# Performance work log

Measured on AMD Instinct MI355X. Metric: run time of the kernel, lower is better.

Reference implementation:

```python
import jax, jax.numpy as jnp
import numpy as np

D_MODEL = 1024
N_HEADS = 16
HEAD_DIM = D_MODEL // N_HEADS
SEQ_LEN = 2048
LN_EPS = 1e-5


def setup_inputs() -> dict:
    key = jax.random.key(0)
    ks = jax.random.split(key, 7)
    s = 1.0 / np.sqrt(D_MODEL)
    h = jax.random.normal(ks[0], (SEQ_LEN, D_MODEL), dtype=jnp.float32)
    # torch nn.Linear weights are (out_features, in_features)
    W_qkv = jax.random.uniform(ks[1], (3 * D_MODEL, D_MODEL), jnp.float32, -s, s)
    b_qkv = jax.random.uniform(ks[2], (3 * D_MODEL,), jnp.float32, -s, s)
    W_out = jax.random.uniform(ks[3], (D_MODEL, D_MODEL), jnp.float32, -s, s)
    b_out = jax.random.uniform(ks[4], (D_MODEL,), jnp.float32, -s, s)
    gamma = jnp.ones((D_MODEL,), jnp.float32)
    beta = jnp.zeros((D_MODEL,), jnp.float32)
    return {"h": h, "W_qkv": W_qkv, "b_qkv": b_qkv, "W_out": W_out,
            "b_out": b_out, "gamma": gamma, "beta": beta}


def reference(h, W_qkv, b_qkv, W_out, b_out, gamma, beta):
    S = h.shape[0]
    # QKV projection: (S, 3*D)
    qkv = h @ W_qkv.T + b_qkv
    q, k, v = jnp.split(qkv, 3, axis=-1)
    # (S, D) -> (H, S, Dh)
    q = q.reshape(S, N_HEADS, HEAD_DIM).transpose(1, 0, 2)
    k = k.reshape(S, N_HEADS, HEAD_DIM).transpose(1, 0, 2)
    v = v.reshape(S, N_HEADS, HEAD_DIM).transpose(1, 0, 2)
    # scaled dot-product attention, non-causal (matches F.sdpa defaults)
    scale = 1.0 / jnp.sqrt(jnp.asarray(HEAD_DIM, dtype=h.dtype))
    scores = jnp.einsum('hqd,hkd->hqk', q, k) * scale  # (H, S, S)
    attn = jax.nn.softmax(scores, axis=-1)
    attn_out = jnp.einsum('hqk,hkd->hqd', attn, v)     # (H, S, Dh)
    attn_out = attn_out.transpose(1, 0, 2).reshape(S, D_MODEL)
    # output projection + residual + LayerNorm
    attn_out = attn_out @ W_out.T + b_out
    x = h + attn_out
    mu = jnp.mean(x, axis=-1, keepdims=True)
    var = jnp.var(x, axis=-1, keepdims=True)
    x_norm = (x - mu) * jax.lax.rsqrt(var + LN_EPS)
    return x_norm * gamma + beta
```

## Files before the change

kernel.cpp:

```cpp
#include <hip/hip_runtime.h>
#include <stdint.h>

#define SEQ 2048
#define DM 1024
#define NH 16
#define DH 64
#define LN_EPS 1e-5f

typedef __bf16 bf16x8 __attribute__((ext_vector_type(8)));
typedef float f32x4 __attribute__((ext_vector_type(4)));
typedef unsigned short u16;
typedef unsigned short u16x8 __attribute__((ext_vector_type(8)));
typedef unsigned int u32;
typedef short s16x4 __attribute__((ext_vector_type(4)));

__device__ __forceinline__ u16 f2bf(float f) {
  unsigned int u = __float_as_uint(f);
  unsigned int r = (u + 0x7fffu + ((u >> 16) & 1u)) >> 16;
  return (u16)r;
}

__device__ __forceinline__ float bf2f(u16 x) {
  return __uint_as_float(((u32)x) << 16);
}

__device__ __forceinline__ u32 packbf(float a, float b) {
  union { __bf16 h[2]; u32 u; } pw;
  pw.h[0] = (__bf16)a; pw.h[1] = (__bf16)b;
  return pw.u;
}

__device__ __forceinline__ float fast_exp2(float x) {
#if __has_builtin(__builtin_amdgcn_exp2f)
  return __builtin_amdgcn_exp2f(x);
#else
  float r;
  asm("v_exp_f32 %0, %1" : "=v"(r) : "v"(x));
  return r;
#endif
}

__device__ __forceinline__ f32x4 mfma16x16x16bf(s16x4 a, s16x4 b, f32x4 c) {
#if __has_builtin(__builtin_amdgcn_mfma_f32_16x16x16bf16_1k)
  return __builtin_amdgcn_mfma_f32_16x16x16bf16_1k(a, b, c, 0, 0, 0);
#else
  asm("v_mfma_f32_16x16x16_bf16 %0, %1, %2, %0" : "+v"(c) : "v"(a), "v"(b));
  return c;
#endif
}

#define GLD_LDS16(gp, lp) __builtin_amdgcn_global_load_lds( \
  (const __attribute__((address_space(1))) void*)(gp),      \
  (__attribute__((address_space(3))) void*)(lp), 16, 0, 0)

__global__ __launch_bounds__(256)
void k_f2bf3(const float* __restrict__ a, u16* __restrict__ oa, int na,
             const float* __restrict__ b, u16* __restrict__ ob, int nb,
             const float* __restrict__ c, u16* __restrict__ oc, int nc) {
  int i = blockIdx.x * 256 + threadIdx.x;
  const float* src;
  u16* dst;
  if (i < na) { src = a; dst = oa; }
  else if (i < na + nb) { src = b; dst = ob; i -= na; }
  else if (i < na + nb + nc) { src = c; dst = oc; i -= na + nb; }
  else return;
  float4 v = reinterpret_cast<const float4*>(src)[i];
  ushort4 o;
  o.x = f2bf(v.x); o.y = f2bf(v.y); o.z = f2bf(v.z); o.w = f2bf(v.w);
  reinterpret_cast<ushort4*>(dst)[i] = o;
}

template <int EPI, int BM, int BN, int XCDW>
__global__ __launch_bounds__(256)
void k_gemm_bt(const u16* __restrict__ A, const u16* __restrict__ B,
               const float* __restrict__ bias,
               u16* __restrict__ outb, u16* __restrict__ outv,
               int M, int N, int K) {
  constexpr int MF = BM / 32, NF = BN / 32;
  constexpr int WM = BM / 2, WN = BN / 2;
  constexpr int NLOAD = BM / 32 + BN / 32;
  __shared__ u16 Alds[2][BM][64];
  __shared__ u16 Blds[2][BN][64];
  const int tid = threadIdx.x;
  const int w = tid >> 6, l = tid & 63, lg = l >> 4, lr = l & 15;
  const int wr = w >> 1, wc = w & 1;

  int bx = blockIdx.x, by = blockIdx.y, bz = blockIdx.z;
  if (XCDW > 0) {
    const int nx = gridDim.x, ny = gridDim.y;
    const int u = bx + nx * (by + ny * bz);
    const int xcd = u & 7, g = u >> 3;
    bx = xcd * XCDW + (g % XCDW);
    const int rem = g / XCDW;
    by = rem % ny;
    bz = rem / ny;
  }

  const int m0 = by * BM, n0 = bx * BN;
  const int KTall = K >> 6;
  const int ktn = KTall / gridDim.z;
  const int kt0 = bz * ktn;

  f32x4 acc[MF][NF] = {};

  const int srow = l >> 3;
  const int scol = ((l & 7) ^ (srow & 7)) * 8;
  auto stage = [&](int buf, int kt) {
    const int k0 = kt << 6;
#pragma unroll
    for (int p = 0; p < BM / 32; ++p) {
      const int rbase = (w * (BM / 32) + p) * 8;
      GLD_LDS16(A + (size_t)(m0 + rbase + srow) * K + k0 + scol, &Alds[buf][rbase][0]);
    }
#pragma unroll
    for (int p = 0; p < BN / 32; ++p) {
      const int rbase = (w * (BN / 32) + p) * 8;
      GLD_LDS16(B + (size_t)(n0 + rbase + srow) * K + k0 + scol, &Blds[buf][rbase][0]);
    }
  };

  auto aread = [&](int buf, int row, int kbyte) -> bf16x8 {
    const int off = row * 128 + (kbyte ^ ((row & 7) << 4));
    return *reinterpret_cast<const bf16x8*>(
        reinterpret_cast<const char*>(&Alds[buf][0][0]) + off);
  };
  auto bread = [&](int buf, int row, int kbyte) -> bf16x8 {
    const int off = row * 128 + (kbyte ^ ((row & 7) << 4));
    return *reinterpret_cast<const bf16x8*>(
        reinterpret_cast<const char*>(&Blds[buf][0][0]) + off);
  };

  auto compute = [&](int buf) {
#pragma unroll
    for (int kk = 0; kk < 2; ++kk) {
      bf16x8 af[MF], bfr[NF];
#pragma unroll
      for (int mi = 0; mi < MF; ++mi)
        af[mi] = aread(buf, wr * WM + mi * 16 + lr, kk * 64 + lg * 16);
#pragma unroll
      for (int ni = 0; ni < NF; ++ni)
        bfr[ni] = bread(buf, wc * WN + ni * 16 + lr, kk * 64 + lg * 16);
#pragma unroll
      for (int mi = 0; mi < MF; ++mi)
#pragma unroll
        for (int ni = 0; ni < NF; ++ni)
          acc[mi][ni] = __builtin_amdgcn_mfma_f32_16x16x32_bf16(af[mi], bfr[ni], acc[mi][ni], 0, 0, 0);
    }
  };

  stage(0, kt0);
  for (int i = 0; i < ktn; ++i) {
    const int cur = i & 1;
    if (i + 1 < ktn) {
      stage(cur ^ 1, kt0 + i + 1);
      if (NLOAD == 6)      asm volatile("s_waitcnt vmcnt(6)" ::: "memory");
      else if (NLOAD == 4) asm volatile("s_waitcnt vmcnt(4)" ::: "memory");
      else                 asm volatile("s_waitcnt vmcnt(0)" ::: "memory");
    } else {
      asm volatile("s_waitcnt vmcnt(0)" ::: "memory");
    }
    __builtin_amdgcn_s_barrier();
    compute(cur);
    __builtin_amdgcn_s_barrier();
  }

  if (EPI == 3) {
    u16* op = outb + (size_t)bz * M * N;
#pragma unroll
    for (int ni = 0; ni < NF; ++ni) {
      const int n = n0 + wc * WN + ni * 16 + lr;
#pragma unroll
      for (int mi = 0; mi < MF; ++mi) {
#pragma unroll
        for (int r = 0; r < 4; ++r) {
          const int m = m0 + wr * WM + mi * 16 + lg * 4 + r;
          op[(size_t)m * N + n] = f2bf(acc[mi][ni][r]);
        }
      }
    }
  } else {
    if (n0 < 2048) {
#pragma unroll
      for (int ni = 0; ni < NF; ++ni) {
        const int n = n0 + wc * WN + ni * 16 + lr;
        const float bn = bias[n];
#pragma unroll
        for (int mi = 0; mi < MF; ++mi) {
#pragma unroll
          for (int r = 0; r < 4; ++r) {
            const int m = m0 + wr * WM + mi * 16 + lg * 4 + r;
            outb[(size_t)m * 2048 + n] = f2bf(acc[mi][ni][r] + bn);
          }
        }
      }
    } else {
#pragma unroll
      for (int ni = 0; ni < NF; ++ni) {
        const int n = n0 + wc * WN + ni * 16 + lr;
        const float bn = bias[n];
#pragma unroll
        for (int mi = 0; mi < MF; ++mi) {
          const int mb = m0 + wr * WM + mi * 16 + lg * 4;
          ushort4 pk;
          pk.x = f2bf(acc[mi][ni][0] + bn);
          pk.y = f2bf(acc[mi][ni][1] + bn);
          pk.z = f2bf(acc[mi][ni][2] + bn);
          pk.w = f2bf(acc[mi][ni][3] + bn);
          *reinterpret_cast<ushort4*>(&outv[(size_t)(n - 2048) * M + mb]) = pk;
        }
      }
    }
  }
}

template <int KSPLIT>
__global__ __launch_bounds__(256)
void k_attn(const u16* __restrict__ qk, const u16* __restrict__ vt,
            u16* __restrict__ Opart, float* __restrict__ lsum_out) {
  __shared__ u16 Klds[2][64 * 64];
  __shared__ u16 Vlds[2][64 * 64];
  const int tid = threadIdx.x;
  const int w = tid >> 6, l = tid & 63, lg = l >> 4, lr = l & 15;

  const int u = blockIdx.x + 16 * (blockIdx.y + NH * blockIdx.z);
  const int xcd = u & 7, g = u >> 3;
  const int h = 2 * xcd + (g / (16 * KSPLIT));
  const int rem = g % (16 * KSPLIT);
  const int sp = rem >> 4;
  const int qb2 = rem & 15;

  constexpr int NT = (SEQ / 64) / KSPLIT;
  const int kb0 = sp * NT;

  bf16x8 qfA[2], qfB[2];
  {
    const size_t qrowA = (size_t)(qb2 * 128 + w * 16 + lr) * 2048 + h * 64;
    qfA[0] = *reinterpret_cast<const bf16x8*>(&qk[qrowA + lg * 8]);
    qfA[1] = *reinterpret_cast<const bf16x8*>(&qk[qrowA + 32 + lg * 8]);
    const size_t qrowB = qrowA + (size_t)64 * 2048;
    qfB[0] = *reinterpret_cast<const bf16x8*>(&qk[qrowB + lg * 8]);
    qfB[1] = *reinterpret_cast<const bf16x8*>(&qk[qrowB + 32 + lg * 8]);
  }

  const int sr0 = w * 16 + (l >> 3);
  const int sc0 = ((l & 7) ^ (sr0 & 7)) * 8;
  const int sr1 = sr0 + 8;
  const int sc1 = ((l & 7) ^ (sr1 & 7)) * 8;
  const u16* kp0 = qk + 1024 + h * 64 + (size_t)(kb0 * 64 + sr0) * 2048 + sc0;
  const u16* kp1 = qk + 1024 + h * 64 + (size_t)(kb0 * 64 + sr1) * 2048 + sc1;
  const u16* vp0 = vt + (size_t)(h * 64 + sr0) * 2048 + kb0 * 64 + sc0;
  const u16* vp1 = vt + (size_t)(h * 64 + sr1) * 2048 + kb0 * 64 + sc1;

  auto stage = [&](int buf) {
    GLD_LDS16(kp0, &Klds[buf][(w * 16) * 64]);
    GLD_LDS16(kp1, &Klds[buf][(w * 16 + 8) * 64]);
    GLD_LDS16(vp0, &Vlds[buf][(w * 16) * 64]);
    GLD_LDS16(vp1, &Vlds[buf][(w * 16 + 8) * 64]);
    kp0 += (size_t)64 * 2048;
    kp1 += (size_t)64 * 2048;
    vp0 += 64;
    vp1 += 64;
  };

  auto kread = [&](int buf, int row, int kbyte) -> bf16x8 {
    const int off = row * 128 + (kbyte ^ ((row & 7) << 4));
    return *reinterpret_cast<const bf16x8*>(
        reinterpret_cast<const char*>(&Klds[buf][0]) + off);
  };

  f32x4 oaccA[4] = {}, oaccB[4] = {};
  f32x4 laccA = {}, laccB = {};
  const float SC = 0.18033688011112042f;
  const s16x4 ONES = {(short)0x3F80, (short)0x3F80, (short)0x3F80, (short)0x3F80};

  stage(0);

  for (int t = 0; t < NT; ++t) {
    const int cur = t & 1;
    if (t + 1 < NT) {
      stage(cur ^ 1);
      asm volatile("s_waitcnt vmcnt(4)" ::: "memory");
    } else {
      asm volatile("s_waitcnt vmcnt(0)" ::: "memory");
    }
    __builtin_amdgcn_s_barrier();

    u32 pawA[4][2], pawB[4][2];
    __builtin_amdgcn_s_setprio(1);
#pragma unroll
    for (int nt = 0; nt < 4; ++nt) {
      bf16x8 kf0 = kread(cur, nt * 16 + lr, lg * 16);
      bf16x8 kf1 = kread(cur, nt * 16 + lr, 64 + lg * 16);
      f32x4 aA = {}, aB = {};
      aA = __builtin_amdgcn_mfma_f32_16x16x32_bf16(kf0, qfA[0], aA, 0, 0, 0);
      aA = __builtin_amdgcn_mfma_f32_16x16x32_bf16(kf1, qfA[1], aA, 0, 0, 0);
      aB = __builtin_amdgcn_mfma_f32_16x16x32_bf16(kf0, qfB[0], aB, 0, 0, 0);
      aB = __builtin_amdgcn_mfma_f32_16x16x32_bf16(kf1, qfB[1], aB, 0, 0, 0);
      float pA[4], pB[4];
#pragma unroll
      for (int r = 0; r < 4; ++r) {
        pA[r] = fast_exp2(aA[r] * SC);
        pB[r] = fast_exp2(aB[r] * SC);
      }
      pawA[nt][0] = packbf(pA[0], pA[1]);
      pawA[nt][1] = packbf(pA[2], pA[3]);
      pawB[nt][0] = packbf(pB[0], pB[1]);
      pawB[nt][1] = packbf(pB[2], pB[3]);
    }

#pragma unroll
    for (int nt = 0; nt < 4; ++nt) {
      union { u32 wd[2]; s16x4 v; } paA, paB;
      paA.wd[0] = pawA[nt][0]; paA.wd[1] = pawA[nt][1];
      paB.wd[0] = pawB[nt][0]; paB.wd[1] = pawB[nt][1];
      laccA = mfma16x16x16bf(paA.v, ONES, laccA);
      laccB = mfma16x16x16bf(paB.v, ONES, laccB);
#pragma unroll
      for (int nd = 0; nd < 4; ++nd) {
        const int row = nd * 16 + lr;
        const int off = row * 128 + ((nt * 32 + lg * 8) ^ ((row & 7) << 4));
        s16x4 vf = *reinterpret_cast<const s16x4*>(
            reinterpret_cast<const char*>(&Vlds[cur][0]) + off);
        oaccA[nd] = mfma16x16x16bf(paA.v, vf, oaccA[nd]);
        oaccB[nd] = mfma16x16x16bf(paB.v, vf, oaccB[nd]);
      }
    }
    __builtin_amdgcn_s_setprio(0);
    __builtin_amdgcn_s_barrier();
  }

  const size_t obase = (size_t)sp * SEQ * DM;
#pragma unroll
  for (int r = 0; r < 4; ++r) {
    const size_t qA = qb2 * 128 + w * 16 + lg * 4 + r;
    const size_t rowA = obase + qA * DM + h * 64;
    const size_t rowB = rowA + (size_t)64 * DM;
#pragma unroll
    for (int nd = 0; nd < 4; ++nd) {
      Opart[rowA + nd * 16 + lr] = f2bf(oaccA[nd][r]);
      Opart[rowB + nd * 16 + lr] = f2bf(oaccB[nd][r]);
    }
  }
  if (lr == 0) {
    const size_t lbase = ((size_t)sp * NH + h) * SEQ + qb2 * 128 + w * 16;
#pragma unroll
    for (int r = 0; r < 4; ++r) {
      lsum_out[lbase + lg * 4 + r] = laccA[r];
      lsum_out[lbase + 64 + lg * 4 + r] = laccB[r];
    }
  }
}

template <int KSPLIT>
__global__ __launch_bounds__(256)
void k_combine(const u16* __restrict__ Opart, const float* __restrict__ lsum,
               u16* __restrict__ attn_out) {
  const int row = blockIdx.x, tid = threadIdx.x;
  const int h = tid >> 4;
  float den = 0.f;
#pragma unroll
  for (int s = 0; s < KSPLIT; ++s)
    den += lsum[((size_t)s * NH + h) * SEQ + row];
  const float inv = 1.f / den;
  float o[4] = {0.f, 0.f, 0.f, 0.f};
#pragma unroll
  for (int s = 0; s < KSPLIT; ++s) {
    const ushort4 v = reinterpret_cast<const ushort4*>(
        Opart + ((size_t)s * SEQ + row) * DM)[tid];
    o[0] += bf2f(v.x); o[1] += bf2f(v.y);
    o[2] += bf2f(v.z); o[3] += bf2f(v.w);
  }
  ushort4 pk;
  pk.x = f2bf(o[0] * inv); pk.y = f2bf(o[1] * inv);
  pk.z = f2bf(o[2] * inv); pk.w = f2bf(o[3] * inv);
  reinterpret_cast<ushort4*>(attn_out + (size_t)row * DM)[tid] = pk;
}

__global__ __launch_bounds__(256)
void k_ln(const float* __restrict__ hin, const u16* __restrict__ pp,
          const float* __restrict__ bout, const float* __restrict__ gamma,
          const float* __restrict__ beta, float* __restrict__ out) {
  const int row = blockIdx.x, tid = threadIdx.x;
  const float4 hv = reinterpret_cast<const float4*>(hin + (size_t)row * DM)[tid];
  const ushort4 p0 = reinterpret_cast<const ushort4*>(pp + (size_t)row * DM)[tid];
  const ushort4 p1 = reinterpret_cast<const ushort4*>(pp + (size_t)(SEQ + row) * DM)[tid];
  const float4 bv = reinterpret_cast<const float4*>(bout)[tid];
  float4 v;
  v.x = hv.x + bf2f(p0.x) + bf2f(p1.x) + bv.x;
  v.y = hv.y + bf2f(p0.y) + bf2f(p1.y) + bv.y;
  v.z = hv.z + bf2f(p0.z) + bf2f(p1.z) + bv.z;
  v.w = hv.w + bf2f(p0.w) + bf2f(p1.w) + bv.w;
  float s = v.x + v.y + v.z + v.w;
  float q = v.x * v.x + v.y * v.y + v.z * v.z + v.w * v.w;
#pragma unroll
  for (int m = 1; m < 64; m <<= 1) { s += __shfl_xor(s, m); q += __shfl_xor(q, m); }
  __shared__ float sh[8];
  const int w = tid >> 6;
  if ((tid & 63) == 0) { sh[w] = s; sh[4 + w] = q; }
  __syncthreads();
  s = sh[0] + sh[1] + sh[2] + sh[3];
  q = sh[4] + sh[5] + sh[6] + sh[7];
  const float mu = s * (1.f / 1024.f);
  const float var = q * (1.f / 1024.f) - mu * mu;
  const float rstd = rsqrtf(var + LN_EPS);
  float4 g = reinterpret_cast<const float4*>(gamma)[tid];
  float4 b = reinterpret_cast<const float4*>(beta)[tid];
  float4 o;
  o.x = (v.x - mu) * rstd * g.x + b.x;
  o.y = (v.y - mu) * rstd * g.y + b.y;
  o.z = (v.z - mu) * rstd * g.z + b.z;
  o.w = (v.w - mu) * rstd * g.w + b.w;
  reinterpret_cast<float4*>(out + (size_t)row * DM)[tid] = o;
}

extern "C" void kernel_launch(void* const* d_in, const int* in_sizes, int n_in,
                              void* d_out, int out_size, void* d_ws, size_t ws_size,
                              hipStream_t stream) {
  const float* h     = (const float*)d_in[0];
  const float* Wqkv  = (const float*)d_in[1];
  const float* bqkv  = (const float*)d_in[2];
  const float* Wout  = (const float*)d_in[3];
  const float* bout  = (const float*)d_in[4];
  const float* gamma = (const float*)d_in[5];
  const float* beta  = (const float*)d_in[6];
  float* out = (float*)d_out;

  char* ws = (char*)d_ws;
  u16* h_bf      = (u16*)(ws);
  u16* Wqkv_bf   = (u16*)(ws + (size_t)4 * 1024 * 1024);
  u16* Wout_bf   = (u16*)(ws + (size_t)10 * 1024 * 1024);
  u16* qk_bf     = (u16*)(ws + (size_t)12 * 1024 * 1024);
  u16* vt_bf     = (u16*)(ws + (size_t)20 * 1024 * 1024);
  u16* attn_bf   = (u16*)(ws + (size_t)24 * 1024 * 1024);
  u16* Opart     = (u16*)(ws + (size_t)28 * 1024 * 1024);
  u16* Opp       = (u16*)(ws + (size_t)44 * 1024 * 1024);
  float* lsums   = (float*)(ws + (size_t)52 * 1024 * 1024);

  const int na = SEQ * DM / 4, nb = 3 * DM * DM / 4, nc = DM * DM / 4;
  k_f2bf3<<<(na + nb + nc + 255) / 256, 256, 0, stream>>>(
      h, h_bf, na, Wqkv, Wqkv_bf, nb, Wout, Wout_bf, nc);

  k_gemm_bt<2, 64, 128, 3><<<dim3(24, 32), 256, 0, stream>>>(
      h_bf, Wqkv_bf, bqkv, qk_bf, vt_bf, SEQ, 3 * DM, DM);

  k_attn<4><<<dim3(16, 16, 4), 256, 0, stream>>>(qk_bf, vt_bf, Opart, lsums);
  k_combine<4><<<SEQ, 256, 0, stream>>>(Opart, lsums, attn_bf);

  k_gemm_bt<3, 64, 64, 2><<<dim3(16, 32, 2), 256, 0, stream>>>(
      attn_bf, Wout_bf, nullptr, Opp, nullptr, SEQ, DM, DM);

  k_ln<<<SEQ, 256, 0, stream>>>(h, Opp, bout, gamma, beta, out);
}
```

Baseline: 83.35 us.

## Fuse split-K attention combine into output-projection GEMM A-operand staging

Removes the separate combine kernel that summed the four split-K attention partials and normalized by the softmax denominator. The new out-projection GEMM loads all four partial O tiles into registers, sums them, scales by a per-row/per-head inverse denominator precomputed into shared memory, and writes the bf16 result into a swizzled LDS A tile. This drops one launch and the write and re-read of the combined attention buffer. In exchange the A loads go through registers rather than direct-to-LDS, with four times the global reads per A tile and extra conversion arithmetic inside the GEMM main loop.

```diff
diff --git a/kernel.cpp b/kernel.cpp
--- a/kernel.cpp
+++ b/kernel.cpp
@@ -164,50 +164,170 @@
     __builtin_amdgcn_s_barrier();
   }
 
-  if (EPI == 3) {
-    u16* op = outb + (size_t)bz * M * N;
+  if (n0 < 2048) {
 #pragma unroll
     for (int ni = 0; ni < NF; ++ni) {
       const int n = n0 + wc * WN + ni * 16 + lr;
+      const float bn = bias[n];
 #pragma unroll
       for (int mi = 0; mi < MF; ++mi) {
 #pragma unroll
         for (int r = 0; r < 4; ++r) {
           const int m = m0 + wr * WM + mi * 16 + lg * 4 + r;
-          op[(size_t)m * N + n] = f2bf(acc[mi][ni][r]);
+          outb[(size_t)m * 2048 + n] = f2bf(acc[mi][ni][r] + bn);
         }
       }
     }
   } else {
-    if (n0 < 2048) {
-#pragma unroll
-      for (int ni = 0; ni < NF; ++ni) {
-        const int n = n0 + wc * WN + ni * 16 + lr;
-        const float bn = bias[n];
-#pragma unroll
-        for (int mi = 0; mi < MF; ++mi) {
-#pragma unroll
-          for (int r = 0; r < 4; ++r) {
-            const int m = m0 + wr * WM + mi * 16 + lg * 4 + r;
-            outb[(size_t)m * 2048 + n] = f2bf(acc[mi][ni][r] + bn);
-          }
-        }
+#pragma unroll
+    for (int ni = 0; ni < NF; ++ni) {
+      const int n = n0 + wc * WN + ni * 16 + lr;
+      const float bn = bias[n];
+#pragma unroll
+      for (int mi = 0; mi < MF; ++mi) {
+        const int mb = m0 + wr * WM + mi * 16 + lg * 4;
+        ushort4 pk;
+        pk.x = f2bf(acc[mi][ni][0] + bn);
+        pk.y = f2bf(acc[mi][ni][1] + bn);
+        pk.z = f2bf(acc[mi][ni][2] + bn);
+        pk.w = f2bf(acc[mi][ni][3] + bn);
+        *reinterpret_cast<ushort4*>(&outv[(size_t)(n - 2048) * M + mb]) = pk;
       }
+    }
+  }
+}
+
+__global__ __launch_bounds__(256)
+void k_outproj(const u16* __restrict__ Opart, const float* __restrict__ lsums,
+               const u16* __restrict__ B, u16* __restrict__ outp,
+               int M, int N, int K) {
+  constexpr int BM = 64, BN = 64, MF = 2, NF = 2, WM = 32, WN = 32;
+  __shared__ u16 Alds[2][BM][64];
+  __shared__ u16 Blds[2][BN][64];
+  __shared__ float invden[64 * 16];
+  const int tid = threadIdx.x;
+  const int w = tid >> 6, l = tid & 63, lg = l >> 4, lr = l & 15;
+  const int wr = w >> 1, wc = w & 1;
+
+  int bx = blockIdx.x, by = blockIdx.y, bz = blockIdx.z;
+  {
+    const int nx = gridDim.x, ny = gridDim.y;
+    const int u = bx + nx * (by + ny * bz);
+    const int xcd = u & 7, g = u >> 3;
+    bx = xcd * 2 + (g % 2);
+    const int rem = g / 2;
+    by = rem % ny;
+    bz = rem / ny;
+  }
+  const int m0 = by * BM, n0 = bx * BN;
+  const int ktn = (K >> 6) / gridDim.z;
+  const int kt0 = bz * ktn;
+
+#pragma unroll
+  for (int j = 0; j < 4; ++j) {
+    const int v = tid * 4 + j;
+    const int row = v >> 4, hh = v & 15;
+    float den = 0.f;
+#pragma unroll
+    for (int s = 0; s < 4; ++s)
+      den += lsums[(size_t)(s * 16 + hh) * SEQ + m0 + row];
+    invden[row * 16 + hh] = 1.f / den;
+  }
+  __syncthreads();
+
+  f32x4 acc[MF][NF] = {};
+
+  const int srow = l >> 3;
+  const int c8 = l & 7;
+  const int scolB = ((l & 7) ^ (srow & 7)) * 8;
+  u16x8 areg[2][4];
+
+  auto stage = [&](int buf, int kt) {
+#pragma unroll
+    for (int p = 0; p < 2; ++p) {
+      const int row = (w * 2 + p) * 8 + srow;
+      const u16* src = Opart + (size_t)(m0 + row) * 1024 + kt * 64 + c8 * 8;
+#pragma unroll
+      for (int s = 0; s < 4; ++s)
+        areg[p][s] = *reinterpret_cast<const u16x8*>(src + (size_t)s * SEQ * 1024);
+    }
+#pragma unroll
+    for (int p = 0; p < 2; ++p) {
+      const int rbase = (w * 2 + p) * 8;
+      GLD_LDS16(B + (size_t)(n0 + rbase + srow) * K + (kt << 6) + scolB,
+                &Blds[buf][rbase][0]);
+    }
+    asm volatile("s_waitcnt vmcnt(2)" ::: "memory");
+#pragma unroll
+    for (int p = 0; p < 2; ++p) {
+      const int row = (w * 2 + p) * 8 + srow;
+      const float inv = invden[row * 16 + kt];
+      u16x8 pk;
+#pragma unroll
+      for (int j = 0; j < 8; ++j) {
+        const float o = bf2f((u16)areg[p][0][j]) + bf2f((u16)areg[p][1][j]) +
+                        bf2f((u16)areg[p][2][j]) + bf2f((u16)areg[p][3][j]);
+        pk[j] = f2bf(o * inv);
+      }
+      char* dst = reinterpret_cast<char*>(&Alds[buf][0][0]) + row * 128 +
+                  ((c8 * 16) ^ ((row & 7) << 4));
+      *reinterpret_cast<u16x8*>(dst) = pk;
+    }
+  };
+
+  auto aread = [&](int buf, int row, int kbyte) -> bf16x8 {
+    const int off = row * 128 + (kbyte ^ ((row & 7) << 4));
+    return *reinterpret_cast<const bf16x8*>(
+        reinterpret_cast<const char*>(&Alds[buf][0][0]) + off);
+  };
+  auto bread = [&](int buf, int row, int kbyte) -> bf16x8 {
+    const int off = row * 128 + (kbyte ^ ((row & 7) << 4));
+    return *reinterpret_cast<const bf16x8*>(
+        reinterpret_cast<const char*>(&Blds[buf][0][0]) + off);
+  };
+
+  auto compute = [&](int buf) {
+#pragma unroll
+    for (int kk = 0; kk < 2; ++kk) {
+      bf16x8 af[MF], bfr[NF];
+#pragma unroll
+      for (int mi = 0; mi < MF; ++mi)
+        af[mi] = aread(buf, wr * WM + mi * 16 + lr, kk * 64 + lg * 16);
+#pragma unroll
+      for (int ni = 0; ni < NF; ++ni)
+        bfr[ni] = bread(buf, wc * WN + ni * 16 + lr, kk * 64 + lg * 16);
+#pragma unroll
+      for (int mi = 0; mi < MF; ++mi)
+#pragma unroll
+        for (int ni = 0; ni < NF; ++ni)
+          acc[mi][ni] = __builtin_amdgcn_mfma_f32_16x16x32_bf16(af[mi], bfr[ni], acc[mi][ni], 0, 0, 0);
+    }
+  };
+
+  stage(0, kt0);
+  for (int i = 0; i < ktn; ++i) {
+    const int cur = i & 1;
+    if (i + 1 < ktn) {
+      stage(cur ^ 1, kt0 + i + 1);
     } else {
-#pragma unroll
-      for (int ni = 0; ni < NF; ++ni) {
-        const int n = n0 + wc * WN + ni * 16 + lr;
-        const float bn = bias[n];
-#pragma unroll
-        for (int mi = 0; mi < MF; ++mi) {
-          const int mb = m0 + wr * WM + mi * 16 + lg * 4;
-          ushort4 pk;
-          pk.x = f2bf(acc[mi][ni][0] + bn);
-          pk.y = f2bf(acc[mi][ni][1] + bn);
-          pk.z = f2bf(acc[mi][ni][2] + bn);
-          pk.w = f2bf(acc[mi][ni][3] + bn);
-          *reinterpret_cast<ushort4*>(&outv[(size_t)(n - 2048) * M + mb]) = pk;
-        }
+      asm volatile("s_waitcnt vmcnt(0)" ::: "memory");
+    }
+    asm volatile("s_waitcnt lgkmcnt(0)" ::: "memory");
+    __builtin_amdgcn_s_barrier();
+    compute(cur);
+    __builtin_amdgcn_s_barrier();
+  }
+
+  u16* op = outp + (size_t)bz * M * N;
+#pragma unroll
+  for (int ni = 0; ni < NF; ++ni) {
+    const int n = n0 + wc * WN + ni * 16 + lr;
+#pragma unroll
+    for (int mi = 0; mi < MF; ++mi) {
+#pragma unroll
+      for (int r = 0; r < 4; ++r) {
+        const int m = m0 + wr * WM + mi * 16 + lg * 4 + r;
+        op[(size_t)m * N + n] = f2bf(acc[mi][ni][r]);
       }
     }
   }
@@ -349,31 +469,6 @@
       lsum_out[lbase + 64 + lg * 4 + r] = laccB[r];
     }
   }
-}
-
-template <int KSPLIT>
-__global__ __launch_bounds__(256)
-void k_combine(const u16* __restrict__ Opart, const float* __restrict__ lsum,
-               u16* __restrict__ attn_out) {
-  const int row = blockIdx.x, tid = threadIdx.x;
-  const int h = tid >> 4;
-  float den = 0.f;
-#pragma unroll
-  for (int s = 0; s < KSPLIT; ++s)
-    den += lsum[((size_t)s * NH + h) * SEQ + row];
-  const float inv = 1.f / den;
-  float o[4] = {0.f, 0.f, 0.f, 0.f};
-#pragma unroll
-  for (int s = 0; s < KSPLIT; ++s) {
-    const ushort4 v = reinterpret_cast<const ushort4*>(
-        Opart + ((size_t)s * SEQ + row) * DM)[tid];
-    o[0] += bf2f(v.x); o[1] += bf2f(v.y);
-    o[2] += bf2f(v.z); o[3] += bf2f(v.w);
-  }
-  ushort4 pk;
-  pk.x = f2bf(o[0] * inv); pk.y = f2bf(o[1] * inv);
-  pk.z = f2bf(o[2] * inv); pk.w = f2bf(o[3] * inv);
-  reinterpret_cast<ushort4*>(attn_out + (size_t)row * DM)[tid] = pk;
 }
 
 __global__ __launch_bounds__(256)
@@ -431,7 +526,6 @@
   u16* Wout_bf   = (u16*)(ws + (size_t)10 * 1024 * 1024);
   u16* qk_bf     = (u16*)(ws + (size_t)12 * 1024 * 1024);
   u16* vt_bf     = (u16*)(ws + (size_t)20 * 1024 * 1024);
-  u16* attn_bf   = (u16*)(ws + (size_t)24 * 1024 * 1024);
   u16* Opart     = (u16*)(ws + (size_t)28 * 1024 * 1024);
   u16* Opp       = (u16*)(ws + (size_t)44 * 1024 * 1024);
   float* lsums   = (float*)(ws + (size_t)52 * 1024 * 1024);
@@ -444,10 +538,9 @@
       h_bf, Wqkv_bf, bqkv, qk_bf, vt_bf, SEQ, 3 * DM, DM);
 
   k_attn<4><<<dim3(16, 16, 4), 256, 0, stream>>>(qk_bf, vt_bf, Opart, lsums);
-  k_combine<4><<<SEQ, 256, 0, stream>>>(Opart, lsums, attn_bf);
-
-  k_gemm_bt<3, 64, 64, 2><<<dim3(16, 32, 2), 256, 0, stream>>>(
-      attn_bf, Wout_bf, nullptr, Opp, nullptr, SEQ, DM, DM);
+
+  k_outproj<<<dim3(16, 32, 2), 256, 0, stream>>>(
+      Opart, lsums, Wout_bf, Opp, SEQ, DM, DM);
 
   k_ln<<<SEQ, 256, 0, stream>>>(h, Opp, bout, gamma, beta, out);
 }
```

Result: slower. 92.63 us (+11.1%).
